# Kernel optimization log

Measured on AMD Instinct MI355X. Metric: run time of the kernel, lower is better.

## Reference

```python
import jax, jax.numpy as jnp
import numpy as np

KS = (0.8, 0.75, 0.667, 0.5)  # pools 500 -> 400 -> 300 -> 200 -> 100 nodes


def gcn(g, h, W, b):
    # torch GCN.forward with p=0: relu(linear(g @ h))
    return jax.nn.relu(jnp.matmul(g, h) @ W.T + b)


def norm_g(g):
    # faithful to torch: [n,n] / [n] broadcasts over the LAST axis (column-normalize)
    return g / jnp.sum(g, axis=1)


def top_k_graph(scores, g, h, k):
    n = g.shape[0]
    kk = max(2, int(k * n))
    values, idx = jax.lax.top_k(scores, kk)  # sorted descending, matches torch.topk
    new_h = h[idx, :] * values[:, None]
    un_g = (g != 0).astype(g.dtype)
    un_g = (jnp.matmul(un_g, un_g) != 0).astype(g.dtype)  # 2-hop connectivity
    un_g = un_g[idx][:, idx]
    return norm_g(un_g), new_h, idx


def setup_inputs() -> dict:
    key = jax.random.key(0)
    ks = jax.random.split(key, 16)
    N, IN_DIM = 500, 32768
    g = (jax.random.uniform(ks[0], (N, N)) < 0.1).astype(jnp.float32)
    h = jax.random.normal(ks[1], (N, IN_DIM), dtype=jnp.float32)
    inp = {
        "g": g,
        "h": h,
        "W_top": jax.random.normal(ks[2], (1, IN_DIM), dtype=jnp.float32) / np.float32(np.sqrt(IN_DIM)),
        "b_top": jnp.zeros((1,), jnp.float32),
    }
    down_dims = [400, 300, 200, 100]
    for i in range(4):
        inp[f"Wp{i}"] = jax.random.normal(ks[3 + i], (1, 1), dtype=jnp.float32)
        inp[f"bp{i}"] = jnp.zeros((1,), jnp.float32)
        inp[f"Wd{i}"] = jax.random.normal(ks[8 + i], (1, down_dims[i]), dtype=jnp.float32) / np.float32(np.sqrt(down_dims[i]))
        inp[f"bd{i}"] = jnp.zeros((1,), jnp.float32)
    return inp


def reference(g, h, W_top, b_top, Wp0, bp0, Wd0, bd0, Wp1, bp1, Wd1, bd1,
              Wp2, bp2, Wd2, bd2, Wp3, bp3, Wd3, bd3):
    Wp = [Wp0, Wp1, Wp2, Wp3]
    bp = [bp0, bp1, bp2, bp3]
    Wd = [Wd0, Wd1, Wd2, Wd3]
    bd = [bd0, bd1, bd2, bd3]
    h = gcn(g, h, W_top, b_top)  # [500, 1]
    h1 = h
    for i in range(4):
        # SAGPool: scores from a tiny GCN(1 -> 1), then topk prune + 2-hop adjacency
        scores = jax.nn.sigmoid(jnp.squeeze(gcn(g, h, Wp[i], bp[i])))  # [n]
        g, h, idx = top_k_graph(scores, g, h, KS[i])
        # down GCN consumes the diagonal matrix built from the pooled 1-feature h
        h = gcn(g, jnp.diag(jnp.squeeze(h)), Wd[i], bd[i])  # [n_i, 1]
        h1 = jnp.concatenate([h1, h], axis=0)
    return h1  # [500+400+300+200+100, 1] = [1500, 1]
```

## Files before the change

kernel.cpp:

```cpp
#include <hip/hip_runtime.h>


#define MS 16
struct P4 { const float* p[4]; };

__device__ __forceinline__ float bitselF(unsigned m, int k, float v) {
    int s = ((int)(m << (31 - k))) >> 31;
    return __int_as_float(s & __float_as_int(v));
}
__device__ __forceinline__ float fbfly(float v) {
#pragma unroll
    for (int o = 32; o; o >>= 1) v += __shfl_xor(v, o);
    return v;
}
__device__ __forceinline__ int ibfly(int v) {
#pragma unroll
    for (int o = 32; o; o >>= 1) v += __shfl_xor(v, o);
    return v;
}
__device__ __forceinline__ float sigm(float x) { return 1.f / (1.f + expf(-x)); }

__device__ __forceinline__ float pwalk16(const unsigned* __restrict__ row,
                                         const float* __restrict__ val) {
    float a = 0.f;
#pragma unroll
    for (int w = 0; w < 16; ++w) {
        unsigned m = row[w];
        while (m) {
            int b = __ffs((int)m) - 1;
            m &= m - 1;
            a += val[(w << 5) + b];
        }
    }
    return a;
}

__device__ __forceinline__ int wrank(const float* __restrict__ sc, float my,
                                     int r, int lane) {
    int cnt = 0;
#pragma unroll
    for (int q = 0; q < 8; ++q) {
        int j = lane + 64 * q;
        float s = sc[j];
        cnt += (s > my) || (s == my && j < r);
    }
    return ibfly(cnt);
}

__global__ __launch_bounds__(1024) void k_dot(const float* __restrict__ h,
        const float* __restrict__ Wt, const float* __restrict__ g,
        float* __restrict__ V, unsigned* __restrict__ MA) {
    int row = blockIdx.x, t = threadIdx.x;
    const float4* h4 = (const float4*)(h + (size_t)row * 32768);
    const float4* w4 = (const float4*)Wt;
    float acc = 0.f;
#pragma unroll
    for (int j = 0; j < 8; ++j) {
        float4 a = h4[t + 1024 * j], b = w4[t + 1024 * j];
        acc = fmaf(a.x, b.x, fmaf(a.y, b.y, fmaf(a.z, b.z, fmaf(a.w, b.w, acc))));
    }
    acc = fbfly(acc);
    __shared__ float red[16];
    if ((t & 63) == 0) red[t >> 6] = acc;
    __syncthreads();
    if (t == 0) {
        float s = 0.f;
        for (int i = 0; i < 16; ++i) s += red[i];
        V[row] = s;
    }
    if (t < 512) {
        float gv = (t < 500) ? g[row * 500 + t] : 0.f;
        unsigned long long bal = __ballot(gv != 0.f);
        if ((t & 63) == 0) {
            int w = t >> 6;
            MA[row * MS + 2 * w] = (unsigned)bal;
            MA[row * MS + 2 * w + 1] = (unsigned)(bal >> 32);
        }
    }
}

__global__ __launch_bounds__(256) void k_row(const unsigned* __restrict__ MA,
        const float* __restrict__ x, const float* __restrict__ c0,
        const float* __restrict__ c1, float* __restrict__ y,
        float* __restrict__ out, int mode) {
    __shared__ float sv[512];
    int t = threadIdx.x;
    sv[t] = (t < 500) ? x[t] : 0.f;
    int t2 = t + 256;
    sv[t2] = (t2 < 500) ? x[t2] : 0.f;
    __syncthreads();
    int wid = t >> 6, lane = t & 63;
    int r = blockIdx.x * 4 + wid;
    float acc = 0.f;
#pragma unroll
    for (int j = 0; j < 8; ++j) {
        unsigned m = MA[r * MS + 2 * j + (lane >> 5)];
        acc += bitselF(m, lane & 31, sv[64 * j + lane]);
    }
    acc = fbfly(acc);
    if (lane == 0) {
        if (mode == 0) {
            float hv = fmaxf(acc + c0[0], 0.f);
            out[r] = hv;
            y[r] = hv;
        } else {
            y[r] = fmaxf(acc * c0[0] + c1[0], 0.f);
        }
    }
}

__global__ __launch_bounds__(256) void k_rh(const unsigned* __restrict__ MA,
        const float* __restrict__ SHg, const float* __restrict__ Zg,
        int* __restrict__ IDXA, float* __restrict__ HSo,
        unsigned* __restrict__ CPP) {
    __shared__ __align__(16) unsigned sMA[8000];
    __shared__ float sz[512];
    int t = threadIdx.x, wid = t >> 6, lane = t & 63;
    for (int q = t; q < 2000; q += 256)
        ((uint4*)sMA)[q] = ((const uint4*)MA)[q];
    if (t < 500) sz[t] = Zg[t];
    else if (t < 512) sz[t] = -1.f;
    int t2 = t + 256;
    if (t2 < 500) sz[t2] = Zg[t2];
    else if (t2 < 512) sz[t2] = -1.f;
    __syncthreads();
    int i = blockIdx.x * 4 + wid;
    float my = sz[i];
    int rank = wrank(sz, my, i, lane);
    if (rank >= 400) return;
    if (lane == 0) {
        IDXA[rank] = i;
        HSo[i] = SHg[i] * sigm(my);
    }
    int part = lane >> 4, w = lane & 15;
    unsigned acc = 0;
    for (int k = part; k < 500; k += 4) {
        unsigned sel = (sMA[i * MS + (k >> 5)] >> (k & 31)) & 1u;
        acc |= sMA[k * MS + w] & (0u - sel);
    }
    acc |= (unsigned)__shfl_xor((int)acc, 16);
    acc |= (unsigned)__shfl_xor((int)acc, 32);
    if (lane < 16) {
        unsigned m500 = (lane < 15) ? 0xffffffffu : 0xfffffu;
        CPP[i * MS + lane] = ~acc & m500;
    }
}

__global__ __launch_bounds__(1024) void k_fin(const int* __restrict__ IDXA,
        const unsigned* __restrict__ CPP, const float* __restrict__ HSo,
        P4 Wp, P4 bp, P4 Wd, P4 bd, float* __restrict__ out) {
    __shared__ __align__(16) unsigned sCP[8000];
    __shared__ float szC[512], svC[512], s2C[512];
    __shared__ float svO[512], s2O[512], shvO[512], sHSo[512], srsO[512];
    __shared__ int sIDXp[2][512];
    __shared__ unsigned sSELp[2][16];
    __shared__ float sS[8];
    __shared__ float stot0, stot1, stotS;
    __shared__ int sFlag;
    int t = threadIdx.x, wid = t >> 6, lane = t & 63;
    for (int q = t; q < 2000; q += 1024)
        ((uint4*)sCP)[q] = ((const uint4*)CPP)[q];
    if (t < 512) {
        sIDXp[0][t] = (t < 400) ? IDXA[t] : 0;
        svO[t] = 0.f;
        s2O[t] = 0.f;
        svC[t] = 0.f;
        srsO[t] = 1.f;
    }
    if (t < 16) {
        sSELp[0][t] = 0u;
        sSELp[1][t] = 0u;
    }
    if (t == 0) sFlag = 0;
    __syncthreads();
    if (t < 400) {
        int i = sIDXp[0][t];
        atomicOr(&sSELp[0][i >> 5], 1u << (i & 31));
    }
    __syncthreads();
    if (t < 400) {
        int i = sIDXp[0][t];
        int cnt = 0;
#pragma unroll
        for (int w = 0; w < 16; ++w) {
            unsigned m = sCP[i * MS + w];
            unsigned sw = sSELp[0][w];
            while (m) {
                int b = __ffs((int)m) - 1;
                m &= m - 1;
                cnt += (sw >> b) & 1;
            }
        }
        float rs = (float)(400 - cnt);
        srsO[i] = rs;
        float su = HSo[i] * Wd.p[0][t] / rs;
        svC[t] = su;
        svO[i] = su;
    }
    __syncthreads();
    if (t < 64) {
        float p = 0.f;
#pragma unroll
        for (int j = 0; j < 8; ++j) p += svC[t * 8 + j];
        p = fbfly(p);
        if (t == 0) stot0 = p;
    }
    __syncthreads();
    int i0 = 0;
    if (t < 400) {
        i0 = sIDXp[0][t];
        float corr = pwalk16(sCP + i0 * MS, svO);
        float h1 = fmaxf(stot0 - corr + bd.p[0][0], 0.f);
        out[500 + t] = h1;
        shvO[i0] = h1;
        float s2 = h1 / srsO[i0];
        s2C[t] = s2;
        s2O[i0] = s2;
    } else if (t < 512) {
        s2C[t] = 0.f;
    }
    __syncthreads();
    if (t < 64) {
        float p = 0.f;
#pragma unroll
        for (int j = 0; j < 8; ++j) p += s2C[t * 8 + j];
        p = fbfly(p);
        if (t == 0) stot1 = p;
    }
    __syncthreads();
    if (t < 400) {
        float c2 = pwalk16(sCP + i0 * MS, s2O);
        szC[t] = fmaxf((stot1 - c2) * Wp.p[1][0] + bp.p[1][0], 0.f);
    } else if (t < 512) {
        szC[t] = -1.f;
    }
    __syncthreads();
    for (int r0 = wid * 2; r0 < 400; r0 += 32) {
        int r1 = r0 + 1;
        float my0 = szC[r0], my1 = szC[r1];
        int cnt = 0;
#pragma unroll
        for (int q = 0; q < 8; ++q) {
            int j = lane + 64 * q;
            float s = szC[j];
            cnt += (s > my0) || (s == my0 && j < r0);
            cnt += ((s > my1) || (s == my1 && j < r1)) << 16;
        }
        cnt = ibfly(cnt);
        if (lane == 0) {
            int c0 = cnt & 0xffff, c1 = cnt >> 16;
            if (c0 < 300) {
                int io = sIDXp[0][r0];
                sIDXp[1][c0] = io;
                sHSo[io] = shvO[io] * sigm(my0);
                atomicOr(&sSELp[1][io >> 5], 1u << (io & 31));
            }
            if (c1 < 300) {
                int io = sIDXp[0][r1];
                sIDXp[1][c1] = io;
                sHSo[io] = shvO[io] * sigm(my1);
                atomicOr(&sSELp[1][io >> 5], 1u << (io & 31));
            }
        }
    }
    __syncthreads();
    unsigned P[16];
    int inew = 0, pc = 0;
    float su_ = 0.f;
    if (t < 300) {
        inew = sIDXp[1][t];
#pragma unroll
        for (int w = 0; w < 16; ++w) P[w] = sSELp[1][w];
        bool alive = true;
        for (int w2 = 0; w2 < 16 && alive; ++w2) {
            unsigned nb = sSELp[0][w2] & ~sCP[inew * MS + w2];
            while (nb) {
                int b = __ffs((int)nb) - 1;
                nb &= nb - 1;
                const unsigned* cj = sCP + (w2 * 32 + b) * MS;
                unsigned orr = 0;
#pragma unroll
                for (int w = 0; w < 16; ++w) {
                    P[w] &= cj[w];
                    orr |= P[w];
                }
                if (!orr) { alive = false; break; }
            }
        }
#pragma unroll
        for (int w = 0; w < 16; ++w) pc += __popc(P[w]);
        if (pc > 0) atomicOr(&sFlag, 1);
        float rs = (float)(300 - pc);
        su_ = sHSo[inew] * Wd.p[1][t] / rs;
    }
    __syncthreads();
    if (t < 300) {
#pragma unroll
        for (int w = 0; w < 16; ++w) sCP[inew * MS + w] = P[w];
        srsO[inew] = (float)(300 - pc);
        svC[t] = su_;
        svO[inew] = su_;
    } else if (t < 512) {
        svC[t] = 0.f;
    }
    __syncthreads();
    if (sFlag == 0) {
        if (t < 64) {
            float p = 0.f;
#pragma unroll
            for (int j = 0; j < 8; ++j) p += svC[t * 8 + j];
            p = fbfly(p);
            if (t == 0) {
                float h2 = fmaxf(p + bd.p[1][0], 0.f);
                float z2 = fmaxf(h2 * Wp.p[2][0] + bp.p[2][0], 0.f);
                sS[0] = h2;
                sS[1] = h2 * sigm(z2);
            }
        }
        __syncthreads();
        float HS2 = sS[1];
        if (t < 512) s2C[t] = (t < 200) ? HS2 * Wd.p[2][t] / 200.f : 0.f;
        __syncthreads();
        if (t < 64) {
            float p = 0.f;
#pragma unroll
            for (int j = 0; j < 8; ++j) p += s2C[t * 8 + j];
            p = fbfly(p);
            if (t == 0) {
                float h3 = fmaxf(p + bd.p[2][0], 0.f);
                float z3 = fmaxf(h3 * Wp.p[3][0] + bp.p[3][0], 0.f);
                sS[2] = h3;
                sS[3] = h3 * sigm(z3);
            }
        }
        __syncthreads();
        float HS3 = sS[3];
        if (t < 512) s2C[t] = (t < 100) ? HS3 * Wd.p[3][t] / 100.f : 0.f;
        __syncthreads();
        if (t < 64) {
            float p = 0.f;
#pragma unroll
            for (int j = 0; j < 8; ++j) p += s2C[t * 8 + j];
            p = fbfly(p);
            if (t == 0) sS[4] = fmaxf(p + bd.p[3][0], 0.f);
        }
        __syncthreads();
        if (t < 300) out[900 + t] = sS[0];
        else if (t < 500) out[1200 + (t - 300)] = sS[2];
        else if (t < 600) out[1400 + (t - 500)] = sS[4];
        return;
    }
    const int kks[3] = {300, 200, 100};
    const int kns[3] = {200, 100, 0};
    const int offs[3] = {900, 1200, 1400};
    for (int l = 1; l <= 3; ++l) {
        const int kk = kks[l - 1], knext = kns[l - 1], off = offs[l - 1];
        const int cur = l & 1, nxt = cur ^ 1;
        if (t < 64) {
            float p = 0.f;
#pragma unroll
            for (int j = 0; j < 8; ++j) p += svC[t * 8 + j];
            p = fbfly(p);
            if (t == 0) stotS = p;
        }
        __syncthreads();
        int i_ = 0;
        if (t < kk) {
            i_ = sIDXp[cur][t];
            float corr = pwalk16(sCP + i_ * MS, svO);
            float hv = fmaxf(stotS - corr + bd.p[l][0], 0.f);
            out[off + t] = hv;
            shvO[i_] = hv;
            float s2 = hv / srsO[i_];
            s2C[t] = s2;
            s2O[i_] = s2;
        } else if (t < 512) {
            s2C[t] = 0.f;
        }
        if (l == 3) break;
        __syncthreads();
        if (t < 64) {
            float p = 0.f;
#pragma unroll
            for (int j = 0; j < 8; ++j) p += s2C[t * 8 + j];
            p = fbfly(p);
            if (t == 0) stotS = p;
        }
        if (t < 16) sSELp[nxt][t] = 0u;
        __syncthreads();
        float z_ = -1.f;
        if (t < kk) {
            float c2 = pwalk16(sCP + i_ * MS, s2O);
            z_ = fmaxf((stotS - c2) * Wp.p[l + 1][0] + bp.p[l + 1][0], 0.f);
        }
        if (t < 512) szC[t] = (t < kk) ? z_ : -1.f;
        __syncthreads();
        for (int r = wid; r < kk; r += 16) {
            float my = szC[r];
            int cnt = wrank(szC, my, r, lane);
            if (lane == 0 && cnt < knext) {
                int io = sIDXp[cur][r];
                sIDXp[nxt][cnt] = io;
                sHSo[io] = shvO[io] * sigm(my);
                atomicOr(&sSELp[nxt][io >> 5], 1u << (io & 31));
            }
        }
        __syncthreads();
        unsigned Q[16];
        int in2 = 0, pc2 = 0;
        float su2_ = 0.f;
        if (t < knext) {
            in2 = sIDXp[nxt][t];
#pragma unroll
            for (int w = 0; w < 16; ++w) Q[w] = sSELp[nxt][w];
            bool alive = true;
            for (int w2 = 0; w2 < 16 && alive; ++w2) {
                unsigned nb = sSELp[cur][w2] & ~sCP[in2 * MS + w2];
                while (nb) {
                    int b = __ffs((int)nb) - 1;
                    nb &= nb - 1;
                    const unsigned* cj = sCP + (w2 * 32 + b) * MS;
                    unsigned orr = 0;
#pragma unroll
                    for (int w = 0; w < 16; ++w) {
                        Q[w] &= cj[w];
                        orr |= Q[w];
                    }
                    if (!orr) { alive = false; break; }
                }
            }
#pragma unroll
            for (int w = 0; w < 16; ++w) pc2 += __popc(Q[w]);
            float rs = (float)(knext - pc2);
            su2_ = sHSo[in2] * Wd.p[l + 1][t] / rs;
        }
        __syncthreads();
        if (t < knext) {
#pragma unroll
            for (int w = 0; w < 16; ++w) sCP[in2 * MS + w] = Q[w];
            srsO[in2] = (float)(knext - pc2);
            svC[t] = su2_;
            svO[in2] = su2_;
        } else if (t < 512) {
            svC[t] = 0.f;
        }
        __syncthreads();
    }
}

extern "C" void kernel_launch(void* const* d_in, const int* in_sizes, int n_in,
                              void* d_out, int out_size, void* d_ws, size_t ws_size,
                              hipStream_t stream) {
    const float* g = (const float*)d_in[0];
    const float* h = (const float*)d_in[1];
    const float* W_top = (const float*)d_in[2];
    const float* b_top = (const float*)d_in[3];
    P4 Wp, bp, Wd, bd;
    for (int i = 0; i < 4; ++i) {
        Wp.p[i] = (const float*)d_in[4 + 4 * i];
        bp.p[i] = (const float*)d_in[5 + 4 * i];
        Wd.p[i] = (const float*)d_in[6 + 4 * i];
        bd.p[i] = (const float*)d_in[7 + 4 * i];
    }
    float* out = (float*)d_out;

    unsigned* wsu = (unsigned*)d_ws;
    float* V = (float*)(wsu + 0);
    float* SHg = (float*)(wsu + 512);
    float* Zg = (float*)(wsu + 1024);
    int* IDXA = (int*)(wsu + 1536);
    float* HSo = (float*)(wsu + 2048);
    unsigned* CPP = wsu + 2560;
    unsigned* MA = wsu + 10560;

    k_dot<<<500, 1024, 0, stream>>>(h, W_top, g, V, MA);
    k_row<<<125, 256, 0, stream>>>(MA, V, b_top, nullptr, SHg, out, 0);
    k_row<<<125, 256, 0, stream>>>(MA, SHg, Wp.p[0], bp.p[0], Zg, nullptr, 1);
    k_rh<<<125, 256, 0, stream>>>(MA, SHg, Zg, IDXA, HSo, CPP);
    k_fin<<<1, 1024, 0, stream>>>(IDXA, CPP, HSo, Wp, bp, Wd, bd, out);
}
```

Before: 58.01 us.

## Fuse rank/2-hop kernel with final kernel via last-block-done atomic counter

Merges k_rh and the single-block k_fin into one 32-block kernel. A global counter, reset in k_dot, is bumped by each block, and the last block to arrive runs the former k_fin work, with CPP/IDXA/HSo exchanged through agent-scope atomic loads and stores. This removes one kernel launch and the gap between the two kernels. The handoff uses relaxed atomics with no explicit release/acquire fence, so it depends on how the hardware orders memory in practice. The rank phase now runs on fewer, larger blocks.

Result: slower. 60.75 us (+4.7%).

```diff
diff --git a/kernel.cpp b/kernel.cpp
--- a/kernel.cpp
+++ b/kernel.cpp
@@ -3,6 +3,25 @@
 
 #define MS 16
 struct P4 { const float* p[4]; };
+
+__device__ __forceinline__ float ald(const float* p) {
+    return __hip_atomic_load(p, __ATOMIC_RELAXED, __HIP_MEMORY_SCOPE_AGENT);
+}
+__device__ __forceinline__ void ast(float* p, float v) {
+    __hip_atomic_store(p, v, __ATOMIC_RELAXED, __HIP_MEMORY_SCOPE_AGENT);
+}
+__device__ __forceinline__ unsigned aldu(const unsigned* p) {
+    return __hip_atomic_load(p, __ATOMIC_RELAXED, __HIP_MEMORY_SCOPE_AGENT);
+}
+__device__ __forceinline__ void astu(unsigned* p, unsigned v) {
+    __hip_atomic_store(p, v, __ATOMIC_RELAXED, __HIP_MEMORY_SCOPE_AGENT);
+}
+__device__ __forceinline__ int aldi(const int* p) {
+    return __hip_atomic_load(p, __ATOMIC_RELAXED, __HIP_MEMORY_SCOPE_AGENT);
+}
+__device__ __forceinline__ void asti(int* p, int v) {
+    __hip_atomic_store(p, v, __ATOMIC_RELAXED, __HIP_MEMORY_SCOPE_AGENT);
+}
 
 __device__ __forceinline__ float bitselF(unsigned m, int k, float v) {
     int s = ((int)(m << (31 - k))) >> 31;
@@ -49,8 +68,10 @@
 
 __global__ __launch_bounds__(1024) void k_dot(const float* __restrict__ h,
         const float* __restrict__ Wt, const float* __restrict__ g,
-        float* __restrict__ V, unsigned* __restrict__ MA) {
+        float* __restrict__ V, unsigned* __restrict__ MA,
+        unsigned* __restrict__ CNT) {
     int row = blockIdx.x, t = threadIdx.x;
+    if (row == 0 && t == 0) astu(CNT, 0u);
     const float4* h4 = (const float4*)(h + (size_t)row * 32768);
     const float4* w4 = (const float4*)Wt;
     float acc = 0.f;
@@ -109,59 +130,61 @@
     }
 }
 
-__global__ __launch_bounds__(256) void k_rh(const unsigned* __restrict__ MA,
+__global__ __launch_bounds__(1024) void k_rhf(const unsigned* __restrict__ MA,
         const float* __restrict__ SHg, const float* __restrict__ Zg,
         int* __restrict__ IDXA, float* __restrict__ HSo,
-        unsigned* __restrict__ CPP) {
+        unsigned* __restrict__ CPP, unsigned* __restrict__ CNT,
+        P4 Wp, P4 bp, P4 Wd, P4 bd, float* __restrict__ out) {
     __shared__ __align__(16) unsigned sMA[8000];
     __shared__ float sz[512];
-    int t = threadIdx.x, wid = t >> 6, lane = t & 63;
-    for (int q = t; q < 2000; q += 256)
-        ((uint4*)sMA)[q] = ((const uint4*)MA)[q];
-    if (t < 500) sz[t] = Zg[t];
-    else if (t < 512) sz[t] = -1.f;
-    int t2 = t + 256;
-    if (t2 < 500) sz[t2] = Zg[t2];
-    else if (t2 < 512) sz[t2] = -1.f;
-    __syncthreads();
-    int i = blockIdx.x * 4 + wid;
-    float my = sz[i];
-    int rank = wrank(sz, my, i, lane);
-    if (rank >= 400) return;
-    if (lane == 0) {
-        IDXA[rank] = i;
-        HSo[i] = SHg[i] * sigm(my);
-    }
-    int part = lane >> 4, w = lane & 15;
-    unsigned acc = 0;
-    for (int k = part; k < 500; k += 4) {
-        unsigned sel = (sMA[i * MS + (k >> 5)] >> (k & 31)) & 1u;
-        acc |= sMA[k * MS + w] & (0u - sel);
-    }
-    acc |= (unsigned)__shfl_xor((int)acc, 16);
-    acc |= (unsigned)__shfl_xor((int)acc, 32);
-    if (lane < 16) {
-        unsigned m500 = (lane < 15) ? 0xffffffffu : 0xfffffu;
-        CPP[i * MS + lane] = ~acc & m500;
-    }
-}
-
-__global__ __launch_bounds__(1024) void k_fin(const int* __restrict__ IDXA,
-        const unsigned* __restrict__ CPP, const float* __restrict__ HSo,
-        P4 Wp, P4 bp, P4 Wd, P4 bd, float* __restrict__ out) {
-    __shared__ __align__(16) unsigned sCP[8000];
     __shared__ float szC[512], svC[512], s2C[512];
     __shared__ float svO[512], s2O[512], shvO[512], sHSo[512], srsO[512];
     __shared__ int sIDXp[2][512];
     __shared__ unsigned sSELp[2][16];
     __shared__ float sS[8];
     __shared__ float stot0, stot1, stotS;
-    __shared__ int sFlag;
+    __shared__ int sFlag, sLast;
     int t = threadIdx.x, wid = t >> 6, lane = t & 63;
     for (int q = t; q < 2000; q += 1024)
-        ((uint4*)sCP)[q] = ((const uint4*)CPP)[q];
+        ((uint4*)sMA)[q] = ((const uint4*)MA)[q];
+    if (t < 512) sz[t] = (t < 500) ? Zg[t] : -1.f;
+    __syncthreads();
+    int i = blockIdx.x * 16 + wid;
+    if (i < 500) {
+        float my = sz[i];
+        int rank = wrank(sz, my, i, lane);
+        if (rank < 400) {
+            if (lane == 0) {
+                asti(&IDXA[rank], i);
+                ast(&HSo[i], SHg[i] * sigm(my));
+            }
+            int part = lane >> 4, w = lane & 15;
+            unsigned acc = 0;
+            for (int k = part; k < 500; k += 4) {
+                unsigned sel = (sMA[i * MS + (k >> 5)] >> (k & 31)) & 1u;
+                acc |= sMA[k * MS + w] & (0u - sel);
+            }
+            acc |= (unsigned)__shfl_xor((int)acc, 16);
+            acc |= (unsigned)__shfl_xor((int)acc, 32);
+            if (lane < 16) {
+                unsigned m500 = (lane < 15) ? 0xffffffffu : 0xfffffu;
+                astu(&CPP[i * MS + lane], ~acc & m500);
+            }
+        }
+    }
+    __syncthreads();
+    if (t == 0) {
+        unsigned old = __hip_atomic_fetch_add(CNT, 1u, __ATOMIC_RELAXED,
+                                              __HIP_MEMORY_SCOPE_AGENT);
+        sLast = (old == 31u);
+    }
+    __syncthreads();
+    if (!sLast) return;
+
+    unsigned* sCP = sMA;
+    for (int q = t; q < 8000; q += 1024) sCP[q] = aldu(&CPP[q]);
     if (t < 512) {
-        sIDXp[0][t] = (t < 400) ? IDXA[t] : 0;
+        sIDXp[0][t] = (t < 400) ? aldi(&IDXA[t]) : 0;
         svO[t] = 0.f;
         s2O[t] = 0.f;
         svC[t] = 0.f;
@@ -174,16 +197,16 @@
     if (t == 0) sFlag = 0;
     __syncthreads();
     if (t < 400) {
-        int i = sIDXp[0][t];
-        atomicOr(&sSELp[0][i >> 5], 1u << (i & 31));
+        int ii = sIDXp[0][t];
+        atomicOr(&sSELp[0][ii >> 5], 1u << (ii & 31));
     }
     __syncthreads();
     if (t < 400) {
-        int i = sIDXp[0][t];
+        int ii = sIDXp[0][t];
         int cnt = 0;
 #pragma unroll
         for (int w = 0; w < 16; ++w) {
-            unsigned m = sCP[i * MS + w];
+            unsigned m = sCP[ii * MS + w];
             unsigned sw = sSELp[0][w];
             while (m) {
                 int b = __ffs((int)m) - 1;
@@ -192,10 +215,10 @@
             }
         }
         float rs = (float)(400 - cnt);
-        srsO[i] = rs;
-        float su = HSo[i] * Wd.p[0][t] / rs;
+        srsO[ii] = rs;
+        float su = ald(&HSo[ii]) * Wd.p[0][t] / rs;
         svC[t] = su;
-        svO[i] = su;
+        svO[ii] = su;
     }
     __syncthreads();
     if (t < 64) {
@@ -470,12 +493,13 @@
     float* Zg = (float*)(wsu + 1024);
     int* IDXA = (int*)(wsu + 1536);
     float* HSo = (float*)(wsu + 2048);
-    unsigned* CPP = wsu + 2560;
-    unsigned* MA = wsu + 10560;
-
-    k_dot<<<500, 1024, 0, stream>>>(h, W_top, g, V, MA);
+    unsigned* CNT = wsu + 2592;
+    unsigned* CPP = wsu + 2624;
+    unsigned* MA = wsu + 10624;
+
+    k_dot<<<500, 1024, 0, stream>>>(h, W_top, g, V, MA, CNT);
     k_row<<<125, 256, 0, stream>>>(MA, V, b_top, nullptr, SHg, out, 0);
     k_row<<<125, 256, 0, stream>>>(MA, SHg, Wp.p[0], bp.p[0], Zg, nullptr, 1);
-    k_rh<<<125, 256, 0, stream>>>(MA, SHg, Zg, IDXA, HSo, CPP);
-    k_fin<<<1, 1024, 0, stream>>>(IDXA, CPP, HSo, Wp, bp, Wd, bd, out);
-}
+    k_rhf<<<32, 1024, 0, stream>>>(MA, SHg, Zg, IDXA, HSo, CPP, CNT,
+                                   Wp, bp, Wd, bd, out);
+}
```
